# Kernel optimization log

Measured on AMD Instinct MI355X. Metric: run time of the kernel, lower is better.

## Reference

```python
import jax, jax.numpy as jnp
import numpy as np

B, T, L = 8, 5, 16          # meta-batch, inner (train) steps, test examples per task
C, H, W = 3, 64, 64
NCLS = 100
FEAT = 256 * (H // 16) * (W // 16)  # 4096
CHANS = [(C, 32), (32, 64), (64, 128), (128, 256), (256, 256)]
DN = ('NCHW', 'OIHW', 'NCHW')


def setup_inputs() -> dict:
    key = jax.random.key(0)
    ks = jax.random.split(key, 16)
    inp = {}
    for j, (ic, oc) in enumerate(CHANS):
        std = 1.0 / np.sqrt(ic * 9)
        inp[f"w{j}"] = jax.random.normal(ks[j], (oc, ic, 3, 3), jnp.float32) * std
        inp[f"b{j}"] = jnp.zeros((oc,), jnp.float32)
    inp["W_out"] = jax.random.normal(ks[5], (NCLS, FEAT), jnp.float32) / np.sqrt(FEAT)
    inp["b_out"] = jnp.zeros((NCLS,), jnp.float32)
    inp["inner_log_lr"] = jnp.asarray(np.log(0.01), jnp.float32)
    inp["train_x"] = jax.random.normal(ks[6], (B, T, C, H, W), jnp.float32)
    inp["test_x"] = jax.random.normal(ks[7], (B, L, C, H, W), jnp.float32)
    inp["train_gate"] = jax.random.uniform(ks[8], (B, T, FEAT), dtype=jnp.float32)
    inp["test_gate"] = jax.random.uniform(ks[9], (B, L, FEAT), dtype=jnp.float32)
    inp["train_y"] = jax.random.randint(ks[10], (B, T), 0, NCLS)
    inp["test_y"] = jax.random.randint(ks[11], (B, L), 0, NCLS)
    inp["evaluate"] = 1
    return inp


def _conv(x, w, b, s):
    # x: [N, C, H, W]; per-example weight w: [OC, IC, 3, 3]; 'same'-ish pad=1
    y = jax.lax.conv_general_dilated(x, w, (s, s), [(1, 1), (1, 1)], dimension_numbers=DN)
    return jax.nn.relu(y + b[None, :, None, None])


def _features(fw, x, gate):
    # x: [B, L, C, H, W]; fw: tuple of per-example (batched) params
    for j in range(5):
        s = 1 if j == 0 else 2
        x = jax.vmap(_conv, in_axes=(0, 0, 0, None))(x, fw[2 * j], fw[2 * j + 1], s)
    return x.reshape(x.shape[0], x.shape[1], -1) * gate  # [B, L, FEAT]


def _ce(logits, y):
    return -jnp.take_along_axis(jax.nn.log_softmax(logits, -1), y[..., None], -1)[..., 0]


def _forward(params, log_lr, train_x, test_x, train_gate, test_gate, train_y, test_y):
    b = train_x.shape[0]
    lr = jnp.exp(log_lr)
    # per-example fast weights (MAML)
    fw = tuple(jnp.broadcast_to(p, (b,) + p.shape) for p in params)

    def step(fw, batch):
        xi, yi, gi = batch  # [B,C,H,W], [B], [B,FEAT]
        def loss_fn(fw):
            f = _features(fw, xi[:, None], gi[:, None])[:, 0]  # [B, FEAT]
            logit = jnp.einsum('bnm,bm->bn', fw[10], f) + fw[11]
            return _ce(logit, yi).sum()
        g = jax.grad(loss_fn)(fw)
        return tuple(w - lr * gw for w, gw in zip(fw, g)), None

    fw, _ = jax.lax.scan(
        step, fw,
        (jnp.swapaxes(train_x, 0, 1), jnp.swapaxes(train_y, 0, 1), jnp.swapaxes(train_gate, 0, 1)))

    f = _features(fw, test_x, test_gate)                         # [B, L, FEAT]
    logit = jnp.einsum('bnm,blm->bln', fw[10], f) + fw[11][:, None, :]
    loss = _ce(logit, test_y)[..., None]                          # [B, L, 1]
    return loss, lr, logit


def reference(w0, b0, w1, b1, w2, b2, w3, b3, w4, b4, W_out, b_out, inner_log_lr,
              train_x, test_x, train_gate, test_gate, train_y, test_y, evaluate):
    params = (w0, b0, w1, b1, w2, b2, w3, b3, w4, b4, W_out, b_out)
    loss, lr, logit = _forward(params, inner_log_lr, train_x, test_x,
                               train_gate, test_gate, train_y, test_y)
    evaluation = (jnp.argmax(logit, -1) == test_y) if evaluate else None
    return (loss, lr, evaluation, logit)
```

## Files before the change

### kernel.cpp

```cpp
#include <hip/hip_runtime.h>

#define NB 8
#define NT 5
#define NL 16
#define NCLS 100
#define FEAT 4096
#define CHW (3*64*64)

#define OFF_W0 0
#define OFF_B0 864
#define OFF_W1 896
#define OFF_B1 19328
#define OFF_W2 19392
#define OFF_B2 93120
#define OFF_W3 93248
#define OFF_B3 388160
#define OFF_W4 388416
#define OFF_B4 978240
#define OFF_WO 978496
#define OFF_BO 1388096
#define PT     1388196

#define A1 0
#define A2 131072
#define A3 196608
#define A4 229376
#define A5 245760
#define ATOT 249856

struct Params12 { const float* p[12]; };

__global__ void bcast_kernel(Params12 ps, float* __restrict__ fw) {
    const int offs[13] = {OFF_W0,OFF_B0,OFF_W1,OFF_B1,OFF_W2,OFF_B2,OFF_W3,OFF_B3,
                          OFF_W4,OFF_B4,OFF_WO,OFF_BO,PT};
    long idx = (long)blockIdx.x * blockDim.x + threadIdx.x;
    long total = (long)NB * PT;
    if (idx >= total) return;
    int i = (int)(idx % PT);
    int j = 11;
    while (j > 0 && i < offs[j]) --j;
    fw[idx] = ps.p[j][i - offs[j]];
}

__global__ void conv_fwd(const float* __restrict__ xb, long x_ts, long x_es,
                         const float* __restrict__ fw, int woff, int boff,
                         float* __restrict__ yb, long y_ts,
                         int N, int IC, int IH, int IW, int OC, int OH, int OW, int s)
{
    long idx = (long)blockIdx.x * blockDim.x + threadIdx.x;
    long total = (long)NB * N * OC * OH * OW;
    if (idx >= total) return;
    int ow = (int)(idx % OW); long r = idx / OW;
    int oh = (int)(r % OH); r /= OH;
    int oc = (int)(r % OC); r /= OC;
    int n  = (int)(r % N);  int b = (int)(r / N);

    const float* x = xb + (long)b * x_ts + (long)n * x_es;
    const float* w = fw + (long)b * PT + woff + (long)oc * IC * 9;
    float acc = fw[(long)b * PT + boff + oc];
    int ih0 = oh * s - 1, iw0 = ow * s - 1;
    for (int ic = 0; ic < IC; ++ic) {
        const float* xc = x + (long)ic * IH * IW;
        const float* wc = w + ic * 9;
        #pragma unroll
        for (int kh = 0; kh < 3; ++kh) {
            int ih = ih0 + kh;
            if (ih < 0 || ih >= IH) continue;
            #pragma unroll
            for (int kw = 0; kw < 3; ++kw) {
                int iw = iw0 + kw;
                if (iw < 0 || iw >= IW) continue;
                acc += xc[ih * IW + iw] * wc[kh * 3 + kw];
            }
        }
    }
    yb[(long)b * y_ts + (((long)n * OC + oc) * OH + oh) * OW + ow] = fmaxf(acc, 0.f);
}

template<int IC,int IH,int IW,int OC,int OH,int OW,int S,int UF,int BS>
__global__ __launch_bounds__(BS) void conv_fwd_u(
    const float* __restrict__ xb, long x_ts,
    const float* __restrict__ fw, int woff, int boff,
    float* __restrict__ yb, long y_ts)
{
    constexpr int OHW = OH*OW, IHW = IH*IW;
    long idx = (long)blockIdx.x * BS + threadIdx.x;
    int pix = (int)(idx % OHW); long r = idx / OHW;
    int oc = (int)(r % OC); int b = (int)(r / OC);
    int oh = pix / OW, ow = pix % OW;
    int ih0 = oh*S - 1, iw0 = ow*S - 1;

    const float* x = xb + (long)b * x_ts;
    const float* w = fw + (long)b * PT + woff + (long)oc * IC * 9;
    float acc = fw[(long)b * PT + boff + oc];

    #pragma unroll 1
    for (int ic0 = 0; ic0 < IC; ic0 += UF) {
        float xv[UF][9];
        #pragma unroll
        for (int u = 0; u < UF; ++u) {
            const float* xc = x + (long)(ic0 + u) * IHW;
            #pragma unroll
            for (int kh = 0; kh < 3; ++kh) {
                int ih = ih0 + kh;
                #pragma unroll
                for (int kw = 0; kw < 3; ++kw) {
                    int iw = iw0 + kw;
                    bool v = ((unsigned)ih < (unsigned)IH) && ((unsigned)iw < (unsigned)IW);
                    xv[u][kh*3+kw] = v ? xc[ih*IW + iw] : 0.f;
                }
            }
        }
        #pragma unroll
        for (int u = 0; u < UF; ++u) {
            const float* wc = w + (ic0 + u) * 9;
            #pragma unroll
            for (int k = 0; k < 9; ++k)
                acc += xv[u][k] * wc[k];
        }
    }
    yb[(long)b * y_ts + (long)oc * OHW + pix] = fmaxf(acc, 0.f);
}

template<int IC,int IH,int IW,int OC,int OH,int OW,int S,int TOC,int NSUB,int ICB>
__global__ __launch_bounds__(256) void conv_fwd2(
    const float* __restrict__ xb, long x_ts, long x_es,
    const float* __restrict__ fw, int woff, int boff,
    float* __restrict__ yb, long y_ts, int N)
{
    constexpr int OHW = OH*OW, IHW = IH*IW;
    constexpr int PPB = 256/NSUB;
    constexpr int TILES = OHW/PPB;
    constexpr int OCB = NSUB*TOC;
    constexpr int NOCG = OC/OCB;
    __shared__ float wlds[ICB*9*OCB];

    int bi = blockIdx.x;
    int tile = bi % TILES;
    int ocg  = (bi / TILES) % NOCG;
    int n    = (bi / (TILES*NOCG)) % N;
    int b    = bi / (TILES*NOCG*N);

    int tid = threadIdx.x;
    int pixl = tid % PPB, sub = tid / PPB;
    int pix = tile * PPB + pixl;
    int oc0 = ocg * OCB + sub * TOC;
    int oh = pix / OW, ow = pix % OW;
    int ih0 = oh*S - 1, iw0 = ow*S - 1;

    const float* xp  = xb + (long)b * x_ts + (long)n * x_es;
    const float* fwp = fw + (long)b * PT + woff;
    const float* bp  = fw + (long)b * PT + boff;

    float acc[TOC];
    #pragma unroll
    for (int t = 0; t < TOC; ++t) acc[t] = bp[oc0 + t];

    #pragma unroll 1
    for (int ic0i = 0; ic0i < IC; ic0i += ICB) {
        __syncthreads();
        for (int i = tid; i < ICB*9*OCB; i += 256) {
            int o = i % OCB; int rem = i / OCB; int k = rem % 9; int icb = rem / 9;
            wlds[i] = fwp[((long)(ocg*OCB + o) * IC + ic0i + icb) * 9 + k];
        }
        __syncthreads();
        #pragma unroll 2
        for (int icb = 0; icb < ICB; ++icb) {
            const float* xc = xp + (long)(ic0i + icb) * IHW;
            float xv[9];
            #pragma unroll
            for (int kh = 0; kh < 3; ++kh)
            #pragma unroll
            for (int kw = 0; kw < 3; ++kw) {
                int ih = ih0 + kh, iw = iw0 + kw;
                bool v = ((unsigned)ih < (unsigned)IH) && ((unsigned)iw < (unsigned)IW);
                xv[kh*3+kw] = v ? xc[ih*IW + iw] : 0.f;
            }
            const float* wl = wlds + icb*9*OCB + sub*TOC;
            #pragma unroll
            for (int k = 0; k < 9; ++k) {
                #pragma unroll
                for (int t = 0; t < TOC; ++t)
                    acc[t] += xv[k] * wl[k*OCB + t];
            }
        }
    }

    float* yp = yb + (long)b * y_ts;
    #pragma unroll
    for (int t = 0; t < TOC; ++t)
        yp[((long)n*OC + oc0 + t) * OHW + pix] = fmaxf(acc[t], 0.f);
}

template<int IC,int IH,int IW,int OC,int OH,int OW,int S,int TOC,int ICB,int NTOT>
__global__ __launch_bounds__(256) void conv_fwd2b(
    const float* __restrict__ xb, long x_ts, long x_es,
    const float* __restrict__ fw, int woff, int boff,
    float* __restrict__ yb, long y_ts)
{
    constexpr int OHW = OH*OW, IHW = IH*IW;
    constexpr int PSP = NTOT*OHW;
    constexpr int TILES = PSP/256;
    constexpr int OCB = TOC;
    constexpr int NOCG = OC/OCB;
    __shared__ float wlds[ICB*9*OCB];

    int bi = blockIdx.x;
    int tile = bi % TILES;
    int ocg  = (bi / TILES) % NOCG;
    int b    = bi / (TILES*NOCG);

    int tid = threadIdx.x;
    int pixg = tile * 256 + tid;
    int n = pixg / OHW, pix = pixg % OHW;
    int oc0 = ocg * OCB;
    int oh = pix / OW, ow = pix % OW;
    int ih0 = oh*S - 1, iw0 = ow*S - 1;

    const float* xp  = xb + (long)b * x_ts + (long)n * x_es;
    const float* fwp = fw + (long)b * PT + woff;
    const float* bp  = fw + (long)b * PT + boff;

    float acc[TOC];
    #pragma unroll
    for (int t = 0; t < TOC; ++t) acc[t] = bp[oc0 + t];

    #pragma unroll 1
    for (int ic0i = 0; ic0i < IC; ic0i += ICB) {
        __syncthreads();
        for (int i = tid; i < ICB*9*OCB; i += 256) {
            int o = i % OCB; int rem = i / OCB; int k = rem % 9; int icb = rem / 9;
            wlds[i] = fwp[((long)(ocg*OCB + o) * IC + ic0i + icb) * 9 + k];
        }
        __syncthreads();
        #pragma unroll 2
        for (int icb = 0; icb < ICB; ++icb) {
            const float* xc = xp + (long)(ic0i + icb) * IHW;
            float xv[9];
            #pragma unroll
            for (int kh = 0; kh < 3; ++kh)
            #pragma unroll
            for (int kw = 0; kw < 3; ++kw) {
                int ih = ih0 + kh, iw = iw0 + kw;
                bool v = ((unsigned)ih < (unsigned)IH) && ((unsigned)iw < (unsigned)IW);
                xv[kh*3+kw] = v ? xc[ih*IW + iw] : 0.f;
            }
            const float* wl = wlds + icb*9*OCB;
            #pragma unroll
            for (int k = 0; k < 9; ++k) {
                #pragma unroll
                for (int t = 0; t < TOC; ++t)
                    acc[t] += xv[k] * wl[k*OCB + t];
            }
        }
    }

    float* yp = yb + (long)b * y_ts;
    #pragma unroll
    for (int t = 0; t < TOC; ++t)
        yp[((long)n*OC + oc0 + t) * OHW + pix] = fmaxf(acc[t], 0.f);
}

template<int IC,int IH,int IW,int OC,int OH,int OW,int S,int TOC,int ICB,int NTOT,int KS>
__global__ __launch_bounds__(256) void conv_fwd2c(
    const float* __restrict__ xb, long x_ts, long x_es,
    const float* __restrict__ fw, int woff,
    float* __restrict__ pb)
{
    constexpr int OHW = OH*OW, IHW = IH*IW;
    constexpr int PSP = NTOT*OHW;
    constexpr int TILES = PSP/256;
    constexpr int OCB = TOC;
    constexpr int NOCG = OC/OCB;
    constexpr int ICC = IC/KS;
    __shared__ float wlds[ICB*9*OCB];

    int bi = blockIdx.x;
    int tile = bi % TILES;
    int ocg  = (bi / TILES) % NOCG;
    int ks   = (bi / (TILES*NOCG)) % KS;
    int b    = bi / (TILES*NOCG*KS);

    int tid = threadIdx.x;
    int pixg = tile * 256 + tid;
    int n = pixg / OHW, pix = pixg % OHW;
    int oc0 = ocg * OCB;
    int oh = pix / OW, ow = pix % OW;
    int ih0 = oh*S - 1, iw0 = ow*S - 1;

    const float* xp  = xb + (long)b * x_ts + (long)n * x_es;
    const float* fwp = fw + (long)b * PT + woff;

    float acc[TOC];
    #pragma unroll
    for (int t = 0; t < TOC; ++t) acc[t] = 0.f;

    const int ic_beg = ks * ICC, ic_end = ic_beg + ICC;
    #pragma unroll 1
    for (int ic0i = ic_beg; ic0i < ic_end; ic0i += ICB) {
        __syncthreads();
        for (int i = tid; i < ICB*9*OCB; i += 256) {
            int o = i % OCB; int rem = i / OCB; int k = rem % 9; int icb = rem / 9;
            wlds[i] = fwp[((long)(ocg*OCB + o) * IC + ic0i + icb) * 9 + k];
        }
        __syncthreads();
        #pragma unroll 2
        for (int icb = 0; icb < ICB; ++icb) {
            const float* xc = xp + (long)(ic0i + icb) * IHW;
            float xv[9];
            #pragma unroll
            for (int kh = 0; kh < 3; ++kh)
            #pragma unroll
            for (int kw = 0; kw < 3; ++kw) {
                int ih = ih0 + kh, iw = iw0 + kw;
                bool v = ((unsigned)ih < (unsigned)IH) && ((unsigned)iw < (unsigned)IW);
                xv[kh*3+kw] = v ? xc[ih*IW + iw] : 0.f;
            }
            const float* wl = wlds + icb*9*OCB;
            #pragma unroll
            for (int k = 0; k < 9; ++k) {
                #pragma unroll
                for (int t = 0; t < TOC; ++t)
                    acc[t] += xv[k] * wl[k*OCB + t];
            }
        }
    }

    float* yp = pb + ((long)ks * NB + b) * ((long)NTOT * OC * OHW);
    #pragma unroll
    for (int t = 0; t < TOC; ++t)
        yp[((long)n*OC + oc0 + t) * OHW + pix] = acc[t];
}

template<int KS>
__global__ __launch_bounds__(256) void ksum_relu(
    const float* __restrict__ pb, const float* __restrict__ fw, int boff,
    float* __restrict__ yb, long y_ts, int N, int OC, int OHW)
{
    long plane = (long)N * OC * OHW;
    long idx = (long)blockIdx.x * 256 + threadIdx.x;
    long total = (long)NB * plane;
    if (idx >= total) return;
    int b = (int)(idx / plane);
    long rem = idx % plane;
    int oc = (int)((rem / OHW) % OC);
    float s = fw[(long)b * PT + boff + oc];
    #pragma unroll
    for (int ks = 0; ks < KS; ++ks)
        s += pb[((long)ks * NB + b) * plane + rem];
    yb[(long)b * y_ts + rem] = fmaxf(s, 0.f);
}

template<int IC,int IH,int IW,int OC,int OH,int OW,int S,int OCT,int ICT,int OCPT,int OHC>
__global__ __launch_bounds__(256) void conv_bwd_dwg(
    float* __restrict__ fw, int woff, int boff,
    const float* __restrict__ dzbuf, int dz_off,
    const float* __restrict__ xb, long x_ts,
    const float* __restrict__ loglr)
{
    constexpr int OHW = OH*OW, IHW = IH*IW;
    constexpr int IW2 = IW + 2;
    constexpr int RW  = OHC*S + 1;
    constexpr int XPRAW = RW * IW2;
    constexpr int XP = XPRAW | 1;
    constexpr int OHWC = OHC*OW;
    constexpr int DZP = OHWC + 1;
    constexpr int NCH = OH/OHC;
    constexpr int OCSL = OCT/OCPT;
    static_assert(OCSL*ICT == 256, "block must be 256 threads");
    static_assert((OW & (OW-1)) == 0, "OW power of two");
    constexpr int LOG_OW = (OW==4) ? 2 : ((OW==8) ? 3 : 4);
    constexpr int NOCG = OC/OCT, NICG = IC/ICT;

    __shared__ float dzs[OCT*DZP];
    __shared__ float xs[ICT*XP];

    int bi = blockIdx.x;
    int icg = bi % NICG;
    int ocg = (bi / NICG) % NOCG;
    int b   = bi / (NICG*NOCG);
    int oc0 = ocg*OCT, ic0 = icg*ICT;

    int tid = threadIdx.x;
    int ic_sub = tid % ICT;
    int oc_sub = tid / ICT;

    const float* dzp = dzbuf + (long)b*ATOT + dz_off + (long)oc0*OHW;
    const float* xp  = xb + (long)b*x_ts + (long)ic0*IHW;

    float acc[OCPT][9];
    float accb[OCPT];
    #pragma unroll
    for (int p = 0; p < OCPT; ++p) {
        accb[p] = 0.f;
        #pragma unroll
        for (int k = 0; k < 9; ++k) acc[p][k] = 0.f;
    }

    for (int c = 0; c < NCH; ++c) {
        if (c) __syncthreads();
        for (int i = tid; i < OCT*OHWC; i += 256) {
            int oc = i / OHWC, j = i % OHWC;
            dzs[oc*DZP + j] = dzp[(long)oc*OHW + c*OHWC + j];
        }
        for (int i = tid; i < ICT*XPRAW; i += 256) {
            int ic = i / XPRAW, j = i % XPRAW;
            int r = j / IW2, col = j % IW2;
            int ih = c*(OHC*S) - 1 + r;
            int iw = col - 1;
            float v = 0.f;
            if ((unsigned)ih < (unsigned)IH && (unsigned)iw < (unsigned)IW)
                v = xp[(long)ic*IHW + ih*IW + iw];
            xs[ic*XP + j] = v;
        }
        __syncthreads();

        const float* dzr = dzs + oc_sub*DZP;
        const float* xr0 = xs + ic_sub*XP;
        #pragma unroll 2
        for (int pos = 0; pos < OHWC; ++pos) {
            int ohl = pos >> LOG_OW;
            int ow  = pos & (OW-1);
            const float* xr = xr0 + (ohl*S)*IW2 + ow*S;
            float xv[9];
            #pragma unroll
            for (int kh = 0; kh < 3; ++kh)
                #pragma unroll
                for (int kw = 0; kw < 3; ++kw)
                    xv[kh*3+kw] = xr[kh*IW2 + kw];
            #pragma unroll
            for (int p = 0; p < OCPT; ++p) {
                float dzv = dzr[p*OCSL*DZP + pos];
                accb[p] += dzv;
                #pragma unroll
                for (int k = 0; k < 9; ++k) acc[p][k] += dzv * xv[k];
            }
        }
    }

    float lr = expf(loglr[0]);
    #pragma unroll
    for (int p = 0; p < OCPT; ++p) {
        int oc = oc0 + p*OCSL + oc_sub;
        float* wp = fw + (long)b*PT + woff + ((long)oc*IC + ic0 + ic_sub)*9;
        #pragma unroll
        for (int k = 0; k < 9; ++k) wp[k] -= lr * acc[p][k];
        if (ic_sub == 0 && icg == 0)
            fw[(long)b*PT + boff + oc] -= lr * accb[p];
    }
}

__global__ void head_fwd(const float* __restrict__ a5b, long a_ts, long a_es,
                         const float* __restrict__ gb, long g_ts, long g_es,
                         const float* __restrict__ fw,
                         float* __restrict__ ob, long o_ts, long o_es, int N)
{
    int wid = (int)(((long)blockIdx.x * blockDim.x + threadIdx.x) >> 6);
    int lane = threadIdx.x & 63;
    int total = NB * N * NCLS;
    if (wid >= total) return;
    int cls = wid % NCLS; int r = wid / NCLS;
    int n = r % N; int b = r / N;
    const float* a5 = a5b + (long)b * a_ts + (long)n * a_es;
    const float* g  = gb  + (long)b * g_ts + (long)n * g_es;
    const float* W  = fw + (long)b * PT + OFF_WO + (long)cls * FEAT;
    float acc = 0.f;
    for (int m = lane; m < FEAT; m += 64) acc += W[m] * a5[m] * g[m];
    for (int off = 32; off; off >>= 1) acc += __shfl_down(acc, off, 64);
    if (lane == 0)
        ob[(long)b * o_ts + (long)n * o_es + cls] = acc + fw[(long)b * PT + OFF_BO + cls];
}

__global__ void softmax_dlogit(const float* __restrict__ logi, const int* __restrict__ ty, int t,
                               float* __restrict__ dlog)
{
    __shared__ float red[128];
    int b = blockIdx.x, tid = threadIdx.x;
    const float* lo = logi + b * NCLS;
    float v = (tid < NCLS) ? lo[tid] : -1e30f;
    red[tid] = v; __syncthreads();
    for (int s2 = 64; s2; s2 >>= 1) { if (tid < s2) red[tid] = fmaxf(red[tid], red[tid + s2]); __syncthreads(); }
    float mx = red[0]; __syncthreads();
    float e = (tid < NCLS) ? expf(v - mx) : 0.f;
    red[tid] = e; __syncthreads();
    for (int s2 = 64; s2; s2 >>= 1) { if (tid < s2) red[tid] += red[tid + s2]; __syncthreads(); }
    float sum = red[0];
    if (tid < NCLS) {
        int y = ty[b * NT + t];
        dlog[b * NCLS + tid] = e / sum - (tid == y ? 1.f : 0.f);
    }
}

__global__ void head_bwd_dz5(const float* __restrict__ fw, const float* __restrict__ dlog,
                             const float* __restrict__ ain, const float* __restrict__ gb, long g_ts,
                             float* __restrict__ dz)
{
    int idx = blockIdx.x * blockDim.x + threadIdx.x;
    if (idx >= NB * FEAT) return;
    int m = idx % FEAT, b = idx / FEAT;
    const float* W = fw + (long)b * PT + OFF_WO;
    float df = 0.f;
    for (int c = 0; c < NCLS; ++c) df += W[(long)c * FEAT + m] * dlog[b * NCLS + c];
    float a = ain[(long)b * ATOT + A5 + m];
    dz[(long)b * ATOT + A5 + m] = (a > 0.f) ? df * gb[(long)b * g_ts + m] : 0.f;
}

__global__ void head_update(float* __restrict__ fw, const float* __restrict__ dlog,
                            const float* __restrict__ ain, const float* __restrict__ gb, long g_ts,
                            const float* __restrict__ loglr)
{
    long idx = (long)blockIdx.x * blockDim.x + threadIdx.x;
    long total = (long)NB * NCLS * FEAT;
    if (idx >= total) return;
    int m = (int)(idx % FEAT); long r = idx / FEAT;
    int c = (int)(r % NCLS); int b = (int)(r / NCLS);
    float lr = expf(loglr[0]);
    float f = ain[(long)b * ATOT + A5 + m] * gb[(long)b * g_ts + m];
    float dl = dlog[b * NCLS + c];
    fw[(long)b * PT + OFF_WO + (long)c * FEAT + m] -= lr * dl * f;
    if (m == 0) fw[(long)b * PT + OFF_BO + c] -= lr * dl;
}

template<int IC,int IH,int IW,int OC,int OH,int OW,int ICG,int BLK>
__global__ __launch_bounds__(BLK) void conv_bwd_dx2(
    const float* __restrict__ dzbuf, int dz_off,
    const float* __restrict__ fw, int woff,
    const float* __restrict__ ain, int ain_off,
    float* __restrict__ dzin, int dzin_off)
{
    constexpr int IHW = IH*IW, OHW = OH*OW, NICG = IC/ICG, PB = IHW/BLK;
    __shared__ float wlds[OC*9*ICG];
    int bi = blockIdx.x;
    int pb  = bi % PB;
    int icg = (bi / PB) % NICG;
    int b   = bi / (PB * NICG);
    int ic0 = icg * ICG;
    const float* fwp = fw + (long)b * PT + woff;
    for (int i = threadIdx.x; i < OC*9*ICG; i += BLK) {
        int g = i % ICG; int rem = i / ICG; int k = rem % 9; int oc = rem / 9;
        wlds[i] = fwp[((long)oc * IC + ic0 + g) * 9 + k];
    }
    __syncthreads();

    int pix = pb * BLK + threadIdx.x;
    int ih = pix / IW, iw = pix % IW;
    int kh0 = (ih + 1) & 1, kw0 = (iw + 1) & 1;
    int ohA = (ih + 1 - kh0) >> 1, owA = (iw + 1 - kw0) >> 1;
    float mhA = (ohA < OH) ? 1.f : 0.f;   float mhB = (kh0 == 0) ? 1.f : 0.f;
    float mwA = (owA < OW) ? 1.f : 0.f;   float mwB = (kw0 == 0) ? 1.f : 0.f;
    int ohB = ohA - 1, owB = owA - 1;
    int ohAc = (ohA < OH) ? ohA : 0;  int owAc = (owA < OW) ? owA : 0;
    int ohBc = (ohB >= 0) ? ohB : 0;  int owBc = (owB >= 0) ? owB : 0;

    int oAA = ohAc*OW + owAc; float mAA = mhA*mwA; int kAA = kh0*3 + kw0;
    int oAB = ohAc*OW + owBc; float mAB = mhA*mwB; int kAB = kh0*3 + kw0 + 2;
    int oBA = ohBc*OW + owAc; float mBA = mhB*mwA; int kBA = (kh0+2)*3 + kw0;
    int oBB = ohBc*OW + owBc; float mBB = mhB*mwB; int kBB = (kh0+2)*3 + kw0 + 2;

    const float* dzp = dzbuf + (long)b * ATOT + dz_off;
    float acc[ICG];
    #pragma unroll
    for (int g = 0; g < ICG; ++g) acc[g] = 0.f;

    for (int oc = 0; oc < OC; ++oc) {
        const float* dzo = dzp + oc * OHW;
        float dAA = dzo[oAA] * mAA;
        float dAB = dzo[oAB] * mAB;
        float dBA = dzo[oBA] * mBA;
        float dBB = dzo[oBB] * mBB;
        const float* w = wlds + oc * 9 * ICG;
        #pragma unroll
        for (int g = 0; g < ICG; ++g)
            acc[g] += dAA * w[kAA*ICG+g] + dAB * w[kAB*ICG+g]
                    + dBA * w[kBA*ICG+g] + dBB * w[kBB*ICG+g];
    }
    #pragma unroll
    for (int g = 0; g < ICG; ++g) {
        long p = (long)b * ATOT + (long)(ic0 + g) * IHW + pix;
        float a = ain[p + ain_off];
        dzin[p + dzin_off] = (a > 0.f) ? acc[g] : 0.f;
    }
}

template<int IC,int IH,int IW,int OC,int OH,int OW,int S>
__global__ __launch_bounds__(64) void conv_bwd_dw2(
    float* __restrict__ fw, int woff, int boff,
    const float* __restrict__ dzbuf, int dz_off,
    const float* __restrict__ xb, long x_ts,
    const float* __restrict__ loglr)
{
    constexpr int OHW = OH*OW;
    int bi = blockIdx.x;
    int ic = bi % IC; int oc = (bi / IC) % OC; int b = bi / (IC * OC);
    int lane = threadIdx.x;
    const float* dzp = dzbuf + (long)b * ATOT + dz_off + (long)oc * OHW;
    const float* xp  = xb + (long)b * x_ts + (long)ic * IH * IW;

    float acc[10];
    #pragma unroll
    for (int k = 0; k < 10; ++k) acc[k] = 0.f;

    for (int pos = lane; pos < OHW; pos += 64) {
        float dzv = dzp[pos];
        int oh = pos / OW, ow = pos % OW;
        int ihb = oh * S - 1, iwb = ow * S - 1;
        acc[9] += dzv;
        #pragma unroll
        for (int kh = 0; kh < 3; ++kh) {
            int ih = ihb + kh;
            bool hv = ((unsigned)ih < (unsigned)IH);
            #pragma unroll
            for (int kw = 0; kw < 3; ++kw) {
                int iw = iwb + kw;
                float xv = (hv && (unsigned)iw < (unsigned)IW) ? xp[ih * IW + iw] : 0.f;
                acc[kh*3+kw] += dzv * xv;
            }
        }
    }
    #pragma unroll
    for (int k = 0; k < 10; ++k)
        for (int off = 32; off; off >>= 1) acc[k] += __shfl_down(acc[k], off, 64);

    if (lane == 0) {
        float lr = expf(loglr[0]);
        float* wp = fw + (long)b * PT + woff + ((long)oc * IC + ic) * 9;
        #pragma unroll
        for (int k = 0; k < 9; ++k) wp[k] -= lr * acc[k];
        if (ic == 0) fw[(long)b * PT + boff + oc] -= lr * acc[9];
    }
}

__global__ void final_loss_eval(const float* __restrict__ logit_base,
                                const int* __restrict__ test_y,
                                float* __restrict__ out, int l0, int Lc)
{
    int idx = blockIdx.x * blockDim.x + threadIdx.x;
    if (idx >= NB * Lc) return;
    int n = idx % Lc, b = idx / Lc;
    int l = l0 + n;
    const float* lo = logit_base + ((long)b * NL + l) * NCLS;
    float mx = -1e30f; int am = 0;
    for (int c = 0; c < NCLS; ++c) { float v = lo[c]; if (v > mx) { mx = v; am = c; } }
    float se = 0.f;
    for (int c = 0; c < NCLS; ++c) se += expf(lo[c] - mx);
    int y = test_y[b * NL + l];
    out[b * NL + l] = -(lo[y] - mx - logf(se));
    out[129 + b * NL + l] = (am == y) ? 1.f : 0.f;
}

__global__ void write_lr(const float* __restrict__ loglr, float* __restrict__ out)
{
    if (threadIdx.x == 0 && blockIdx.x == 0) out[128] = expf(loglr[0]);
}

extern "C" void kernel_launch(void* const* d_in, const int* in_sizes, int n_in,
                              void* d_out, int out_size, void* d_ws, size_t ws_size,
                              hipStream_t stream)
{
    const float* loglr      = (const float*)d_in[12];
    const float* train_x    = (const float*)d_in[13];
    const float* test_x     = (const float*)d_in[14];
    const float* train_gate = (const float*)d_in[15];
    const float* test_gate  = (const float*)d_in[16];
    const int*   train_y    = (const int*)d_in[17];
    const int*   test_y     = (const int*)d_in[18];
    float* out = (float*)d_out;

    const long base = (long)NB*PT + 2L*NB*ATOT + 2L*NB*NCLS;
    int LCr = 4;
    if (ws_size >= (size_t)(base + 16L*1572864) * 4) LCr = 16;
    else if (ws_size >= (size_t)(base + 8L*1572864) * 4) LCr = 8;

    float* ws   = (float*)d_ws;
    float* FWp  = ws;
    float* AINp = FWp  + (long)NB * PT;
    float* DZp  = AINp + (long)NB * ATOT;
    float* LOGIp= DZp  + (long)NB * ATOT;
    float* DLOGp= LOGIp + NB * NCLS;
    float* TAp  = DLOGp + NB * NCLS;
    float* TBp  = TAp + (long)NB * LCr * 131072;

    Params12 ps;
    for (int j = 0; j < 12; ++j) ps.p[j] = (const float*)d_in[j];
    {
        long tot = (long)NB * PT;
        bcast_kernel<<<(int)((tot + 255) / 256), 256, 0, stream>>>(ps, FWp);
    }

    for (int t = 0; t < NT; ++t) {
        conv_fwd_u<3,64,64,32,64,64,1,3,256><<<4096, 256, 0, stream>>>(
            train_x + (long)t * CHW, (long)NT * CHW, FWp, OFF_W0, OFF_B0, AINp + A1, (long)ATOT);
        conv_fwd_u<32,64,64,64,32,32,2,4,256><<<2048, 256, 0, stream>>>(
            AINp + A1, (long)ATOT, FWp, OFF_W1, OFF_B1, AINp + A2, (long)ATOT);
        conv_fwd_u<64,32,32,128,16,16,2,4,256><<<1024, 256, 0, stream>>>(
            AINp + A2, (long)ATOT, FWp, OFF_W2, OFF_B2, AINp + A3, (long)ATOT);
        conv_fwd_u<128,16,16,256,8,8,2,4,64><<<2048, 64, 0, stream>>>(
            AINp + A3, (long)ATOT, FWp, OFF_W3, OFF_B3, AINp + A4, (long)ATOT);
        conv_fwd_u<256,8,8,256,4,4,2,8,64><<<512, 64, 0, stream>>>(
            AINp + A4, (long)ATOT, FWp, OFF_W4, OFF_B4, AINp + A5, (long)ATOT);

        {
            long waves = (long)NB * NCLS;
            head_fwd<<<(int)((waves * 64 + 255) / 256), 256, 0, stream>>>(
                AINp + A5, (long)ATOT, 0,
                train_gate + (long)t * FEAT, (long)NT * FEAT, 0,
                FWp, LOGIp, (long)NCLS, 0, 1);
        }
        softmax_dlogit<<<NB, 128, 0, stream>>>(LOGIp, train_y, t, DLOGp);
        head_bwd_dz5<<<(NB * FEAT + 255) / 256, 256, 0, stream>>>(
            FWp, DLOGp, AINp, train_gate + (long)t * FEAT, (long)NT * FEAT, DZp);
        {
            long tot = (long)NB * NCLS * FEAT;
            head_update<<<(int)((tot + 255) / 256), 256, 0, stream>>>(
                FWp, DLOGp, AINp, train_gate + (long)t * FEAT, (long)NT * FEAT, loglr);
        }

        conv_bwd_dx2<256,8,8,256,4,4,2,64><<<8*128, 64, 0, stream>>>(
            DZp, A5, FWp, OFF_W4, AINp, A4, DZp, A4);
        conv_bwd_dwg<256,8,8,256,4,4,2, 64,8,2, 4><<<1024, 256, 0, stream>>>(
            FWp, OFF_W4, OFF_B4, DZp, A5, AINp + A4, (long)ATOT, loglr);

        conv_bwd_dx2<128,16,16,256,8,8,4,256><<<8*32, 256, 0, stream>>>(
            DZp, A4, FWp, OFF_W3, AINp, A3, DZp, A3);
        conv_bwd_dwg<128,16,16,256,8,8,2, 64,8,2, 8><<<512, 256, 0, stream>>>(
            FWp, OFF_W3, OFF_B3, DZp, A4, AINp + A3, (long)ATOT, loglr);

        conv_bwd_dx2<64,32,32,128,16,16,4,256><<<8*16*4, 256, 0, stream>>>(
            DZp, A3, FWp, OFF_W2, AINp, A2, DZp, A2);
        conv_bwd_dwg<64,32,32,128,16,16,2, 32,8,1, 4><<<256, 256, 0, stream>>>(
            FWp, OFF_W2, OFF_B2, DZp, A3, AINp + A2, (long)ATOT, loglr);

        conv_bwd_dx2<32,64,64,64,32,32,4,256><<<8*8*16, 256, 0, stream>>>(
            DZp, A2, FWp, OFF_W1, AINp, A1, DZp, A1);
        conv_bwd_dw2<32,64,64,64,32,32,2><<<8*64*32, 64, 0, stream>>>(
            FWp, OFF_W1, OFF_B1, DZp, A2, AINp + A1, (long)ATOT, loglr);
        conv_bwd_dw2<3,64,64,32,64,64,1><<<8*32*3, 64, 0, stream>>>(
            FWp, OFF_W0, OFF_B0, DZp, A1, train_x + (long)t * CHW, (long)NT * CHW, loglr);
    }

    if (LCr == 16) {
        conv_fwd2<3,64,64,32,64,64,1, 32,1,3><<<NB*16*16, 256, 0, stream>>>(
            test_x, (long)NL * CHW, CHW,
            FWp, OFF_W0, OFF_B0, TAp, 16L * 131072, 16);
        conv_fwd2<32,64,64,64,32,32,2, 16,1,8><<<NB*16*16, 256, 0, stream>>>(
            TAp, 16L * 131072, 131072,
            FWp, OFF_W1, OFF_B1, TBp, 16L * 65536, 16);
        conv_fwd2<64,32,32,128,16,16,2, 16,1,8><<<NB*16*8, 256, 0, stream>>>(
            TBp, 16L * 65536, 65536,
            FWp, OFF_W2, OFF_B2, TAp, 16L * 32768, 16);

        {
            float* P3 = TAp + 4194304;
            conv_fwd2c<128,16,16,256,8,8,2, 16,8,16, 2><<<NB*2*16*4, 256, 0, stream>>>(
                TAp, 16L * 32768, 32768, FWp, OFF_W3, P3);
            ksum_relu<2><<<(int)(((long)NB*16*256*64 + 255) / 256), 256, 0, stream>>>(
                P3, FWp, OFF_B3, TBp, 16L * 16384, 16, 256, 64);
        }
        {
            float* P4 = TBp + 2097152;
            conv_fwd2c<256,8,8,256,4,4,2, 16,8,16, 4><<<NB*4*16*1, 256, 0, stream>>>(
                TBp, 16L * 16384, 16384, FWp, OFF_W4, P4);
            ksum_relu<4><<<(int)(((long)NB*16*256*16 + 255) / 256), 256, 0, stream>>>(
                P4, FWp, OFF_B4, TAp, 16L * 4096, 16, 256, 16);
        }
        {
            long waves = (long)NB * 16 * NCLS;
            head_fwd<<<(int)((waves * 64 + 255) / 256), 256, 0, stream>>>(
                TAp, 16L * FEAT, FEAT,
                test_gate, (long)NL * FEAT, FEAT,
                FWp, out + 257, (long)NL * NCLS, NCLS, 16);
        }
    } else {
        for (int c = 0; c < NL / LCr; ++c) {
            int l0 = c * LCr;
            conv_fwd2<3,64,64,32,64,64,1, 32,1,3><<<NB*LCr*16, 256, 0, stream>>>(
                test_x + (long)l0 * CHW, (long)NL * CHW, CHW,
                FWp, OFF_W0, OFF_B0, TAp, (long)LCr * 131072, LCr);
            conv_fwd2<32,64,64,64,32,32,2, 16,1,8><<<NB*LCr*16, 256, 0, stream>>>(
                TAp, (long)LCr * 131072, 131072,
                FWp, OFF_W1, OFF_B1, TBp, (long)LCr * 65536, LCr);
            conv_fwd2<64,32,32,128,16,16,2, 16,1,8><<<NB*LCr*8, 256, 0, stream>>>(
                TBp, (long)LCr * 65536, 65536,
                FWp, OFF_W2, OFF_B2, TAp, (long)LCr * 32768, LCr);
            conv_fwd2<128,16,16,256,8,8,2, 8,4,8><<<NB*LCr*8, 256, 0, stream>>>(
                TAp, (long)LCr * 32768, 32768,
                FWp, OFF_W3, OFF_B3, TBp, (long)LCr * 16384, LCr);
            conv_fwd2<256,8,8,256,4,4,2, 4,16,8><<<NB*LCr*4, 256, 0, stream>>>(
                TBp, (long)LCr * 16384, 16384,
                FWp, OFF_W4, OFF_B4, TAp, (long)LCr * 4096, LCr);
            {
                long waves = (long)NB * LCr * NCLS;
                head_fwd<<<(int)((waves * 64 + 255) / 256), 256, 0, stream>>>(
                    TAp, (long)LCr * FEAT, FEAT,
                    test_gate + (long)l0 * FEAT, (long)NL * FEAT, FEAT,
                    FWp, out + 257 + (long)l0 * NCLS, (long)NL * NCLS, NCLS, LCr);
            }
        }
    }
    final_loss_eval<<<(NB * NL + 255) / 256, 256, 0, stream>>>(
        out + 257, test_y, out, 0, NL);
    write_lr<<<1, 1, 0, stream>>>(loglr, out);
}
```

Measured before the change: 4.242 ms.

## Split-K the small late-layer convs and first-layer weight gradient for more parallelism

The train-step forward for conv layers 3 and 4 now splits the input-channel reduction across 2 and 4 partial kernels, writing partial sums that a ksum_relu pass reduces and adds bias to. The layer-0 weight gradient is split over 8 spatial chunks, and a finalize kernel sums the partials and applies the SGD update. The test-path split factors for layers 3 and 4 are doubled. The aim is to fill more compute units on these small, under-parallelised kernels, at the cost of extra launches and partial-buffer traffic. It also deletes the unused legacy conv kernels.

```diff
diff --git a/kernel.cpp b/kernel.cpp
--- a/kernel.cpp
+++ b/kernel.cpp
@@ -42,41 +42,6 @@
     fw[idx] = ps.p[j][i - offs[j]];
 }
 
-__global__ void conv_fwd(const float* __restrict__ xb, long x_ts, long x_es,
-                         const float* __restrict__ fw, int woff, int boff,
-                         float* __restrict__ yb, long y_ts,
-                         int N, int IC, int IH, int IW, int OC, int OH, int OW, int s)
-{
-    long idx = (long)blockIdx.x * blockDim.x + threadIdx.x;
-    long total = (long)NB * N * OC * OH * OW;
-    if (idx >= total) return;
-    int ow = (int)(idx % OW); long r = idx / OW;
-    int oh = (int)(r % OH); r /= OH;
-    int oc = (int)(r % OC); r /= OC;
-    int n  = (int)(r % N);  int b = (int)(r / N);
-
-    const float* x = xb + (long)b * x_ts + (long)n * x_es;
-    const float* w = fw + (long)b * PT + woff + (long)oc * IC * 9;
-    float acc = fw[(long)b * PT + boff + oc];
-    int ih0 = oh * s - 1, iw0 = ow * s - 1;
-    for (int ic = 0; ic < IC; ++ic) {
-        const float* xc = x + (long)ic * IH * IW;
-        const float* wc = w + ic * 9;
-        #pragma unroll
-        for (int kh = 0; kh < 3; ++kh) {
-            int ih = ih0 + kh;
-            if (ih < 0 || ih >= IH) continue;
-            #pragma unroll
-            for (int kw = 0; kw < 3; ++kw) {
-                int iw = iw0 + kw;
-                if (iw < 0 || iw >= IW) continue;
-                acc += xc[ih * IW + iw] * wc[kh * 3 + kw];
-            }
-        }
-    }
-    yb[(long)b * y_ts + (((long)n * OC + oc) * OH + oh) * OW + ow] = fmaxf(acc, 0.f);
-}
-
 template<int IC,int IH,int IW,int OC,int OH,int OW,int S,int UF,int BS>
 __global__ __launch_bounds__(BS) void conv_fwd_u(
     const float* __restrict__ xb, long x_ts,
@@ -122,6 +87,53 @@
     yb[(long)b * y_ts + (long)oc * OHW + pix] = fmaxf(acc, 0.f);
 }
 
+template<int IC,int IH,int IW,int OC,int OH,int OW,int S,int UF,int BS,int KS>
+__global__ __launch_bounds__(BS) void conv_fwd_uks(
+    const float* __restrict__ xb, long x_ts,
+    const float* __restrict__ fw, int woff,
+    float* __restrict__ pb)
+{
+    constexpr int OHW = OH*OW, IHW = IH*IW;
+    constexpr int ICC = IC/KS;
+    long idx = (long)blockIdx.x * BS + threadIdx.x;
+    int pix = (int)(idx % OHW); long r = idx / OHW;
+    int oc = (int)(r % OC); r /= OC;
+    int ks = (int)(r % KS); int b = (int)(r / KS);
+    int oh = pix / OW, ow = pix % OW;
+    int ih0 = oh*S - 1, iw0 = ow*S - 1;
+
+    const float* x = xb + (long)b * x_ts;
+    const float* w = fw + (long)b * PT + woff + (long)oc * IC * 9;
+    float acc = 0.f;
+
+    #pragma unroll 1
+    for (int ic0 = ks*ICC; ic0 < (ks+1)*ICC; ic0 += UF) {
+        float xv[UF][9];
+        #pragma unroll
+        for (int u = 0; u < UF; ++u) {
+            const float* xc = x + (long)(ic0 + u) * IHW;
+            #pragma unroll
+            for (int kh = 0; kh < 3; ++kh) {
+                int ih = ih0 + kh;
+                #pragma unroll
+                for (int kw = 0; kw < 3; ++kw) {
+                    int iw = iw0 + kw;
+                    bool v = ((unsigned)ih < (unsigned)IH) && ((unsigned)iw < (unsigned)IW);
+                    xv[u][kh*3+kw] = v ? xc[ih*IW + iw] : 0.f;
+                }
+            }
+        }
+        #pragma unroll
+        for (int u = 0; u < UF; ++u) {
+            const float* wc = w + (ic0 + u) * 9;
+            #pragma unroll
+            for (int k = 0; k < 9; ++k)
+                acc += xv[u][k] * wc[k];
+        }
+    }
+    pb[((long)ks*NB + b) * ((long)OC*OHW) + (long)oc*OHW + pix] = acc;
+}
+
 template<int IC,int IH,int IW,int OC,int OH,int OW,int S,int TOC,int NSUB,int ICB>
 __global__ __launch_bounds__(256) void conv_fwd2(
     const float* __restrict__ xb, long x_ts, long x_es,
@@ -177,75 +189,6 @@
                 xv[kh*3+kw] = v ? xc[ih*IW + iw] : 0.f;
             }
             const float* wl = wlds + icb*9*OCB + sub*TOC;
-            #pragma unroll
-            for (int k = 0; k < 9; ++k) {
-                #pragma unroll
-                for (int t = 0; t < TOC; ++t)
-                    acc[t] += xv[k] * wl[k*OCB + t];
-            }
-        }
-    }
-
-    float* yp = yb + (long)b * y_ts;
-    #pragma unroll
-    for (int t = 0; t < TOC; ++t)
-        yp[((long)n*OC + oc0 + t) * OHW + pix] = fmaxf(acc[t], 0.f);
-}
-
-template<int IC,int IH,int IW,int OC,int OH,int OW,int S,int TOC,int ICB,int NTOT>
-__global__ __launch_bounds__(256) void conv_fwd2b(
-    const float* __restrict__ xb, long x_ts, long x_es,
-    const float* __restrict__ fw, int woff, int boff,
-    float* __restrict__ yb, long y_ts)
-{
-    constexpr int OHW = OH*OW, IHW = IH*IW;
-    constexpr int PSP = NTOT*OHW;
-    constexpr int TILES = PSP/256;
-    constexpr int OCB = TOC;
-    constexpr int NOCG = OC/OCB;
-    __shared__ float wlds[ICB*9*OCB];
-
-    int bi = blockIdx.x;
-    int tile = bi % TILES;
-    int ocg  = (bi / TILES) % NOCG;
-    int b    = bi / (TILES*NOCG);
-
-    int tid = threadIdx.x;
-    int pixg = tile * 256 + tid;
-    int n = pixg / OHW, pix = pixg % OHW;
-    int oc0 = ocg * OCB;
-    int oh = pix / OW, ow = pix % OW;
-    int ih0 = oh*S - 1, iw0 = ow*S - 1;
-
-    const float* xp  = xb + (long)b * x_ts + (long)n * x_es;
-    const float* fwp = fw + (long)b * PT + woff;
-    const float* bp  = fw + (long)b * PT + boff;
-
-    float acc[TOC];
-    #pragma unroll
-    for (int t = 0; t < TOC; ++t) acc[t] = bp[oc0 + t];
-
-    #pragma unroll 1
-    for (int ic0i = 0; ic0i < IC; ic0i += ICB) {
-        __syncthreads();
-        for (int i = tid; i < ICB*9*OCB; i += 256) {
-            int o = i % OCB; int rem = i / OCB; int k = rem % 9; int icb = rem / 9;
-            wlds[i] = fwp[((long)(ocg*OCB + o) * IC + ic0i + icb) * 9 + k];
-        }
-        __syncthreads();
-        #pragma unroll 2
-        for (int icb = 0; icb < ICB; ++icb) {
-            const float* xc = xp + (long)(ic0i + icb) * IHW;
-            float xv[9];
-            #pragma unroll
-            for (int kh = 0; kh < 3; ++kh)
-            #pragma unroll
-            for (int kw = 0; kw < 3; ++kw) {
-                int ih = ih0 + kh, iw = iw0 + kw;
-                bool v = ((unsigned)ih < (unsigned)IH) && ((unsigned)iw < (unsigned)IW);
-                xv[kh*3+kw] = v ? xc[ih*IW + iw] : 0.f;
-            }
-            const float* wl = wlds + icb*9*OCB;
             #pragma unroll
             for (int k = 0; k < 9; ++k) {
                 #pragma unroll
@@ -630,6 +573,74 @@
     }
 }
 
+template<int IC,int IH,int IW,int OC,int OH,int OW,int S,int NSP>
+__global__ __launch_bounds__(64) void conv_bwd_dw2s(
+    float* __restrict__ pbuf,
+    const float* __restrict__ dzbuf, int dz_off,
+    const float* __restrict__ xb, long x_ts)
+{
+    constexpr int OHW = OH*OW, CH = OHW/NSP;
+    int bi = blockIdx.x;
+    int sp = bi % NSP; int ic = (bi / NSP) % IC;
+    int oc = (bi / (NSP*IC)) % OC; int b = bi / (NSP*IC*OC);
+    int lane = threadIdx.x;
+    const float* dzp = dzbuf + (long)b * ATOT + dz_off + (long)oc * OHW;
+    const float* xp  = xb + (long)b * x_ts + (long)ic * IH * IW;
+
+    float acc[10];
+    #pragma unroll
+    for (int k = 0; k < 10; ++k) acc[k] = 0.f;
+
+    for (int pos = sp*CH + lane; pos < sp*CH + CH; pos += 64) {
+        float dzv = dzp[pos];
+        int oh = pos / OW, ow = pos % OW;
+        int ihb = oh * S - 1, iwb = ow * S - 1;
+        acc[9] += dzv;
+        #pragma unroll
+        for (int kh = 0; kh < 3; ++kh) {
+            int ih = ihb + kh;
+            bool hv = ((unsigned)ih < (unsigned)IH);
+            #pragma unroll
+            for (int kw = 0; kw < 3; ++kw) {
+                int iw = iwb + kw;
+                float xv = (hv && (unsigned)iw < (unsigned)IW) ? xp[ih * IW + iw] : 0.f;
+                acc[kh*3+kw] += dzv * xv;
+            }
+        }
+    }
+    #pragma unroll
+    for (int k = 0; k < 10; ++k)
+        for (int off = 32; off; off >>= 1) acc[k] += __shfl_down(acc[k], off, 64);
+
+    if (lane == 0) {
+        float* pp = pbuf + ((((long)sp*NB + b)*OC + oc)*IC + ic)*10;
+        #pragma unroll
+        for (int k = 0; k < 10; ++k) pp[k] = acc[k];
+    }
+}
+
+template<int NSP>
+__global__ void dw_finalize(const float* __restrict__ pbuf, float* __restrict__ fw,
+                            int woff, int boff, const float* __restrict__ loglr,
+                            int OC, int IC)
+{
+    int idx = blockIdx.x * blockDim.x + threadIdx.x;
+    int total = NB * OC * IC * 10;
+    if (idx >= total) return;
+    int k = idx % 10; int r = idx / 10;
+    int ic = r % IC; r /= IC;
+    int oc = r % OC; int b = r / OC;
+    float s = 0.f;
+    #pragma unroll
+    for (int sp = 0; sp < NSP; ++sp)
+        s += pbuf[((((long)sp*NB + b)*OC + oc)*IC + ic)*10 + k];
+    float lr = expf(loglr[0]);
+    if (k < 9)
+        fw[(long)b*PT + woff + ((long)oc*IC + ic)*9 + k] -= lr * s;
+    else if (ic == 0)
+        fw[(long)b*PT + boff + oc] -= lr * s;
+}
+
 __global__ void final_loss_eval(const float* __restrict__ logit_base,
                                 const int* __restrict__ test_y,
                                 float* __restrict__ out, int l0, int Lc)
@@ -680,6 +691,10 @@
     float* TAp  = DLOGp + NB * NCLS;
     float* TBp  = TAp + (long)NB * LCr * 131072;
 
+    float* P3t = TAp;
+    float* P4t = TAp + 262144;
+    float* PW0 = TAp + 262144 + 131072;
+
     Params12 ps;
     for (int j = 0; j < 12; ++j) ps.p[j] = (const float*)d_in[j];
     {
@@ -694,10 +709,14 @@
             AINp + A1, (long)ATOT, FWp, OFF_W1, OFF_B1, AINp + A2, (long)ATOT);
         conv_fwd_u<64,32,32,128,16,16,2,4,256><<<1024, 256, 0, stream>>>(
             AINp + A2, (long)ATOT, FWp, OFF_W2, OFF_B2, AINp + A3, (long)ATOT);
-        conv_fwd_u<128,16,16,256,8,8,2,4,64><<<2048, 64, 0, stream>>>(
-            AINp + A3, (long)ATOT, FWp, OFF_W3, OFF_B3, AINp + A4, (long)ATOT);
-        conv_fwd_u<256,8,8,256,4,4,2,8,64><<<512, 64, 0, stream>>>(
-            AINp + A4, (long)ATOT, FWp, OFF_W4, OFF_B4, AINp + A5, (long)ATOT);
+        conv_fwd_uks<128,16,16,256,8,8,2,4,64, 2><<<4096, 64, 0, stream>>>(
+            AINp + A3, (long)ATOT, FWp, OFF_W3, P3t);
+        ksum_relu<2><<<(NB*256*64 + 255) / 256, 256, 0, stream>>>(
+            P3t, FWp, OFF_B3, AINp + A4, (long)ATOT, 1, 256, 64);
+        conv_fwd_uks<256,8,8,256,4,4,2,8,64, 4><<<2048, 64, 0, stream>>>(
+            AINp + A4, (long)ATOT, FWp, OFF_W4, P4t);
+        ksum_relu<4><<<(NB*256*16 + 255) / 256, 256, 0, stream>>>(
+            P4t, FWp, OFF_B4, AINp + A5, (long)ATOT, 1, 256, 16);
 
         {
             long waves = (long)NB * NCLS;
@@ -734,8 +753,10 @@
             DZp, A2, FWp, OFF_W1, AINp, A1, DZp, A1);
         conv_bwd_dw2<32,64,64,64,32,32,2><<<8*64*32, 64, 0, stream>>>(
             FWp, OFF_W1, OFF_B1, DZp, A2, AINp + A1, (long)ATOT, loglr);
-        conv_bwd_dw2<3,64,64,32,64,64,1><<<8*32*3, 64, 0, stream>>>(
-            FWp, OFF_W0, OFF_B0, DZp, A1, train_x + (long)t * CHW, (long)NT * CHW, loglr);
+        conv_bwd_dw2s<3,64,64,32,64,64,1, 8><<<8*32*3*8, 64, 0, stream>>>(
+            PW0, DZp, A1, train_x + (long)t * CHW, (long)NT * CHW);
+        dw_finalize<8><<<(NB*32*3*10 + 255) / 256, 256, 0, stream>>>(
+            PW0, FWp, OFF_W0, OFF_B0, loglr, 32, 3);
     }
 
     if (LCr == 16) {
@@ -751,16 +772,16 @@
 
         {
             float* P3 = TAp + 4194304;
-            conv_fwd2c<128,16,16,256,8,8,2, 16,8,16, 2><<<NB*2*16*4, 256, 0, stream>>>(
+            conv_fwd2c<128,16,16,256,8,8,2, 16,8,16, 4><<<NB*4*16*4, 256, 0, stream>>>(
                 TAp, 16L * 32768, 32768, FWp, OFF_W3, P3);
-            ksum_relu<2><<<(int)(((long)NB*16*256*64 + 255) / 256), 256, 0, stream>>>(
+            ksum_relu<4><<<(int)(((long)NB*16*256*64 + 255) / 256), 256, 0, stream>>>(
                 P3, FWp, OFF_B3, TBp, 16L * 16384, 16, 256, 64);
         }
         {
             float* P4 = TBp + 2097152;
-            conv_fwd2c<256,8,8,256,4,4,2, 16,8,16, 4><<<NB*4*16*1, 256, 0, stream>>>(
+            conv_fwd2c<256,8,8,256,4,4,2, 16,8,16, 8><<<NB*8*16*1, 256, 0, stream>>>(
                 TBp, 16L * 16384, 16384, FWp, OFF_W4, P4);
-            ksum_relu<4><<<(int)(((long)NB*16*256*16 + 255) / 256), 256, 0, stream>>>(
+            ksum_relu<8><<<(int)(((long)NB*16*256*16 + 255) / 256), 256, 0, stream>>>(
                 P4, FWp, OFF_B4, TAp, 16L * 4096, 16, 256, 16);
         }
         {
```

Measured after the change: 4.100 ms. 3.3% less time.
